# Kernel tuning notes

Measured on AMD Instinct MI355X. Metric: run time of the kernel, lower is better.

The kernel has to match this reference:

```python
import jax, jax.numpy as jnp
import numpy as np
from jax import lax

RADII = (0.1, 0.2, 0.4)
NSAMPLES = (16, 32, 128)
MLPS = ((3, 32, 32, 64), (3, 64, 64, 128), (3, 64, 96, 128))  # divide_ratio=1


def fps(xyz, npoint):
    # iterative farthest point sampling; xyz [B,N,3] -> idx [B,npoint]
    B, N, _ = xyz.shape
    def body(carry, _):
        mind, last = carry
        p = jnp.take_along_axis(xyz, last[:, None, None], axis=1)  # [B,1,3]
        d = jnp.sum((xyz - p) ** 2, -1)
        mind = jnp.minimum(mind, d)
        nxt = jnp.argmax(mind, -1).astype(jnp.int32)
        return (mind, nxt), last
    init = (jnp.full((B, N), 1e10, xyz.dtype), jnp.zeros((B,), jnp.int32))
    _, idx = lax.scan(body, init, None, length=npoint)
    return jnp.transpose(idx)  # [B,npoint]


def ball_query(radius, nsample, xyz, new_xyz):
    # first-nsample neighbors within radius; pad with first valid index
    N = xyz.shape[1]
    sq = jnp.sum((new_xyz[:, :, None, :] - xyz[:, None, :, :]) ** 2, -1)  # [B,S,N]
    cand = jnp.where(sq < radius * radius,
                     jnp.arange(N, dtype=jnp.int32)[None, None, :], N)
    idx = jnp.sort(cand, axis=-1)[:, :, :nsample]
    first = idx[:, :, :1]
    return jnp.where(idx == N, first, idx).astype(jnp.int32)


def scale_branch(xyz, new_xyz, radius, nsample, weights):
    idx = ball_query(radius, nsample, xyz, new_xyz)
    grouped = jax.vmap(lambda x, i: x[i])(xyz, idx)          # [B,S,ns,3]
    h = grouped - new_xyz[:, :, None, :]                      # relative coords (points=None)
    for w, b in weights:                                      # shared 1x1-conv MLP
        h = jax.nn.relu(jnp.einsum('bsnc,co->bsno', h, w) + b)
    return jnp.max(h, axis=2)                                 # maxpool over neighbors [B,S,C]


def _forward(pcd, params, wf, bf):
    npoint = pcd.shape[1] // 8
    idx = fps(pcd, npoint)
    new_xyz = jnp.take_along_axis(pcd, idx[:, :, None], axis=1)  # [B,S,3]
    feats = [scale_branch(pcd, new_xyz, RADII[i], NSAMPLES[i], params[i]) for i in range(3)]
    h = jnp.concatenate(feats, axis=-1)                          # [B,S,320]
    return jnp.einsum('bsc,co->bso', h, wf) + bf                 # patch values [B,S,1]


def setup_inputs() -> dict:
    key = jax.random.key(0)
    ks = jax.random.split(key, 32)
    B, N = 8, 4096
    inp = {"pcd": jax.random.uniform(ks[0], (B, N, 3), jnp.float32)}
    ki = 1
    for si, dims in enumerate(MLPS):
        for li in range(3):
            cin, cout = dims[li], dims[li + 1]
            inp[f"w{si}{li}"] = jax.random.normal(ks[ki], (cin, cout), jnp.float32) * (2.0 / cin) ** 0.5
            inp[f"b{si}{li}"] = jnp.zeros((cout,), jnp.float32)
            ki += 1
    inp["wf"] = jax.random.normal(ks[ki], (320, 1), jnp.float32) * 0.05
    inp["bf"] = jnp.zeros((1,), jnp.float32)
    return inp


def reference(pcd, w00, b00, w01, b01, w02, b02,
              w10, b10, w11, b11, w12, b12,
              w20, b20, w21, b21, w22, b22, wf, bf):
    params = [[(w00, b00), (w01, b01), (w02, b02)],
              [(w10, b10), (w11, b11), (w12, b12)],
              [(w20, b20), (w21, b21), (w22, b22)]]
    return _forward(pcd, params, wf, bf)
```

## Files before the change

kernel.cpp:

```cpp
#include <hip/hip_runtime.h>

#define BATCH 8
#define NPTS 4096
#define NSAMP 512

#define ROW_SHR(n) (0x110 | (n))
#define ROW_BCAST15 0x142
#define ROW_BCAST31 0x143

template <int CTRL, int RMASK>
__device__ __forceinline__ float fmax_dpp(float x) {
  int t = __builtin_amdgcn_update_dpp(0, __float_as_int(x), CTRL, RMASK, 0xf, true);
  return fmaxf(x, __int_as_float(t));
}

__device__ __forceinline__ float wave_max(float x) {
  x = fmax_dpp<ROW_SHR(1), 0xf>(x);
  x = fmax_dpp<ROW_SHR(2), 0xf>(x);
  x = fmax_dpp<ROW_SHR(4), 0xf>(x);
  x = fmax_dpp<ROW_SHR(8), 0xf>(x);
  x = fmax_dpp<ROW_BCAST15, 0xa>(x);
  x = fmax_dpp<ROW_BCAST31, 0xc>(x);
  return x;
}

__device__ __forceinline__ void tsec(int g, const float* __restrict__ w,
                                     float* __restrict__ wt, int cin, int cinp,
                                     int cout, int base) {
  int local = g - base;
  if (local < 0 || local >= cinp * cout) return;
  int oc = local / cinp, ic = local % cinp;
  wt[base + local] = (ic < cin) ? w[ic * cout + oc] : 0.0f;
}

#define W00 0
#define W01 128
#define W02 1152
#define W10 3200
#define W11 3456
#define W12 7552
#define W20 15744
#define WT_TOTAL 16000

__global__ __launch_bounds__(256) void prep_kernel(
    const float* w00, const float* w01, const float* w02,
    const float* w10, const float* w11, const float* w12,
    const float* w20, float* __restrict__ wt) {
  int g = blockIdx.x * 256 + threadIdx.x;
  tsec(g, w00, wt, 3, 4, 32, W00);
  tsec(g, w01, wt, 32, 32, 32, W01);
  tsec(g, w02, wt, 32, 32, 64, W02);
  tsec(g, w10, wt, 3, 4, 64, W10);
  tsec(g, w11, wt, 64, 64, 64, W11);
  tsec(g, w12, wt, 64, 64, 128, W12);
  tsec(g, w20, wt, 3, 4, 64, W20);
}

template <int TOC, int TN>
__device__ __forceinline__ void ib(float (&acc)[TOC][TN], const float* bias) {
#pragma unroll
  for (int j = 0; j < TOC; ++j) {
    float bj = bias[j];
#pragma unroll
    for (int i = 0; i < TN; ++i) acc[j][i] = bj;
  }
}

template <int CIN4, int TOC, int TN, int NTPI, int WS>
__device__ __forceinline__ void layer_acc(const float* __restrict__ wtb,
                                          const float* hin,
                                          float (&acc)[TOC][TN], int tn) {
#pragma unroll 2
  for (int c4 = 0; c4 < CIN4; ++c4) {
    float hv[4][TN];
#pragma unroll
    for (int k = 0; k < 4; ++k) {
      const float* src = &hin[(c4 * 4 + k) * NTPI + tn * TN];
      if constexpr (TN == 1) {
        hv[k][0] = src[0];
      } else if constexpr (TN == 2) {
        float2 v = *(const float2*)src; hv[k][0] = v.x; hv[k][1] = v.y;
      } else {
        float4 v = *(const float4*)src;
        hv[k][0] = v.x; hv[k][1] = v.y; hv[k][2] = v.z; hv[k][3] = v.w;
      }
    }
#pragma unroll
    for (int j = 0; j < TOC; ++j) {
      float4 w4 = *(const float4*)&wtb[j * WS + c4 * 4];
#pragma unroll
      for (int i = 0; i < TN; ++i) {
        acc[j][i] = fmaf(hv[0][i], w4.x, acc[j][i]);
        acc[j][i] = fmaf(hv[1][i], w4.y, acc[j][i]);
        acc[j][i] = fmaf(hv[2][i], w4.z, acc[j][i]);
        acc[j][i] = fmaf(hv[3][i], w4.w, acc[j][i]);
      }
    }
  }
}

template <int TOC, int TN, int NTPO>
__device__ __forceinline__ void store_relu(float* hout,
                                           float (&acc)[TOC][TN], int tn) {
#pragma unroll
  for (int j = 0; j < TOC; ++j) {
    float* dst = &hout[j * NTPO + tn * TN];
    if constexpr (TN == 1) {
      dst[0] = fmaxf(acc[j][0], 0.0f);
    } else if constexpr (TN == 2) {
      *(float2*)dst = make_float2(fmaxf(acc[j][0], 0.0f),
                                  fmaxf(acc[j][1], 0.0f));
    } else {
      *(float4*)dst = make_float4(fmaxf(acc[j][0], 0.0f),
                                  fmaxf(acc[j][1], 0.0f),
                                  fmaxf(acc[j][2], 0.0f),
                                  fmaxf(acc[j][3], 0.0f));
    }
  }
}

template <int TOC, int TN>
__device__ __forceinline__ void rmax_upd(float (&r)[TOC],
                                         float (&acc)[TOC][TN]) {
#pragma unroll
  for (int j = 0; j < TOC; ++j) {
    float m = 0.0f;
#pragma unroll
    for (int i = 0; i < TN; ++i) m = fmaxf(m, acc[j][i]);
    r[j] = fmaxf(r[j], m);
  }
}

template <int TOC>
__device__ __forceinline__ void rmax_commit(float* fdst, float (&r)[TOC],
                                            int tn) {
#pragma unroll
  for (int j = 0; j < TOC; ++j) {
    float v = r[j];
    v = fmaxf(v, __shfl_xor(v, 1));
    v = fmaxf(v, __shfl_xor(v, 2));
    v = fmaxf(v, __shfl_xor(v, 4));
    v = fmaxf(v, __shfl_xor(v, 8));
    if (tn == 0) fdst[j] = v;
  }
}

__global__ __launch_bounds__(256) void fused_kernel(
    const float* __restrict__ pcd, float* __restrict__ new_xyz,
    int* __restrict__ ctrl, const float* __restrict__ wt,
    const float* __restrict__ w21o, const float* __restrict__ w22o,
    const float* __restrict__ b00, const float* __restrict__ b01,
    const float* __restrict__ b02, const float* __restrict__ b10,
    const float* __restrict__ b11, const float* __restrict__ b12,
    const float* __restrict__ b20, const float* __restrict__ b21,
    const float* __restrict__ b22,
    const float* __restrict__ wf, const float* __restrict__ bf,
    float* __restrict__ out) {
  __shared__ __align__(16) float lds[11264];
  __shared__ int s_ticket;

  const int tid = threadIdx.x;
  int* progress = ctrl + 8;

  if (tid == 0) s_ticket = atomicAdd(&ctrl[0], 1);
  __syncthreads();
  const int ticket = s_ticket;

  if (ticket < BATCH) {
    const int b = ticket;
    const int t = tid;
    const int wave = t >> 6, lane = t & 63;
    const float* xb = pcd + (size_t)b * NPTS * 3;
    float4* slot = (float4*)lds;

    float X[16], Y[16], Z[16], mind[16];
    {
      float f[48];
      float4* vv = (float4*)f;
      const float4* src = (const float4*)xb + t * 12;
#pragma unroll
      for (int q = 0; q < 12; ++q) vv[q] = src[q];
#pragma unroll
      for (int j = 0; j < 16; ++j) {
        X[j] = f[3 * j + 0]; Y[j] = f[3 * j + 1]; Z[j] = f[3 * j + 2];
        mind[j] = 10000000000.0f;
      }
    }
    float px = xb[0], py = xb[1], pz = xb[2];

    for (int it = 0; it < NSAMP; ++it) {
      if (t == 0) {
        int* dst = (int*)(new_xyz + ((size_t)b * NSAMP + it) * 3);
        atomicExch(&dst[0], __float_as_int(px));
        atomicExch(&dst[1], __float_as_int(py));
        atomicExch(&dst[2], __float_as_int(pz));
        if ((it & 7) == 7)
          __hip_atomic_store(&progress[b], it + 1, __ATOMIC_RELEASE,
                             __HIP_MEMORY_SCOPE_AGENT);
      }
      float bv = -1.0f, bx = 0.0f, by = 0.0f, bz = 0.0f;
#pragma unroll
      for (int j = 0; j < 16; ++j) {
        float dx = __fsub_rn(X[j], px);
        float dy = __fsub_rn(Y[j], py);
        float dz = __fsub_rn(Z[j], pz);
        float d = __fadd_rn(__fadd_rn(__fmul_rn(dx, dx), __fmul_rn(dy, dy)),
                            __fmul_rn(dz, dz));
        float m = fminf(mind[j], d);
        mind[j] = m;
        bool g = m > bv;
        bv = g ? m : bv;
        bx = g ? X[j] : bx; by = g ? Y[j] : by; bz = g ? Z[j] : bz;
      }
      float wmax = __int_as_float(
          __builtin_amdgcn_readlane(__float_as_int(wave_max(bv)), 63));
      unsigned long long msk = __ballot(bv == wmax);
      if (lane == __ffsll(msk) - 1)
        slot[(it & 1) * 4 + wave] = make_float4(bx, by, bz, wmax);
      __syncthreads();
      float4 cur = slot[(it & 1) * 4 + 0];
#pragma unroll
      for (int w = 1; w < 4; ++w) {
        float4 sw = slot[(it & 1) * 4 + w];
        if (sw.w > cur.w) cur = sw;
      }
      px = cur.x; py = cur.y; pz = cur.z;
    }
    return;
  }

  const int tk = ticket - BATCH;
  const int b = tk & 7;
  const int s = tk >> 3;
  const int bs = (b << 9) | s;
  const int lane = tid & 63;
  const int wave = tid >> 6;
  const int tn = tid & 15, toc = tid >> 4;
  const float* xb = pcd + (size_t)b * NPTS * 3;

  float* h1 = lds;
  float* h2 = lds + 4096;
  float* sB = lds + 4096;
  float* sA = lds + 6272;
  float* cbuf  = lds + 10240;
  float* cbuf2 = lds + 10512;
  float* feat = lds + 10784;
  unsigned long long* masks = (unsigned long long*)(lds + 10784);
  unsigned short* gl = (unsigned short*)(lds + 11168);
  float* bc = lds + 11256;

  if (tid == 0) {
    while (__hip_atomic_load(&progress[b], __ATOMIC_ACQUIRE,
                             __HIP_MEMORY_SCOPE_AGENT) <= s)
      __builtin_amdgcn_s_sleep(2);
    const int* src = (const int*)(new_xyz + (size_t)bs * 3);
    bc[0] = __int_as_float(__hip_atomic_load(&src[0], __ATOMIC_RELAXED,
                                             __HIP_MEMORY_SCOPE_AGENT));
    bc[1] = __int_as_float(__hip_atomic_load(&src[1], __ATOMIC_RELAXED,
                                             __HIP_MEMORY_SCOPE_AGENT));
    bc[2] = __int_as_float(__hip_atomic_load(&src[2], __ATOMIC_RELAXED,
                                             __HIP_MEMORY_SCOPE_AGENT));
  }
  __syncthreads();
  const float cx = bc[0], cy = bc[1], cz = bc[2];

  const float r2a = (float)(0.1 * 0.1);
  const float r2b = (float)(0.2 * 0.2);
  const float r2c = (float)(0.4 * 0.4);
#pragma unroll 4
  for (int j = 0; j < 16; ++j) {
    int i = (j << 8) | tid;
    const float* p = xb + i * 3;
    float dx = __fsub_rn(cx, p[0]);
    float dy = __fsub_rn(cy, p[1]);
    float dz = __fsub_rn(cz, p[2]);
    float sq = __fadd_rn(__fadd_rn(__fmul_rn(dx, dx), __fmul_rn(dy, dy)),
                         __fmul_rn(dz, dz));
    unsigned long long m0 = __ballot(sq < r2a);
    unsigned long long m1 = __ballot(sq < r2b);
    unsigned long long m2 = __ballot(sq < r2c);
    if (lane == 0) {
      int c = (j << 2) | wave;
      masks[0 * 64 + c] = m0; masks[1 * 64 + c] = m1; masks[2 * 64 + c] = m2;
    }
  }
  __syncthreads();

  if (wave < 3) {
    const int ns  = (wave == 0) ? 16 : (wave == 1) ? 32 : 128;
    const int off = (wave == 0) ? 0  : (wave == 1) ? 16 : 48;
    unsigned long long m = masks[wave * 64 + lane];
    int pc = (int)__popcll(m);
    int incl = pc;
#pragma unroll
    for (int o = 1; o < 64; o <<= 1) {
      int u = __shfl_up(incl, o);
      if (lane >= o) incl += u;
    }
    int ex = incl - pc;
    int total = __shfl(incl, 63);
    unsigned short* glw = gl + off;
    unsigned long long mm = m;
    int p = ex;
    while (mm && p < ns) {
      int l = (int)__builtin_ctzll(mm);
      mm &= mm - 1;
      glw[p++] = (unsigned short)((lane << 6) | l);
    }
    int cnt = total < ns ? total : ns;
    unsigned long long nz = __ballot(pc > 0);
    int fl = __ffsll(nz) - 1;
    int myf = (lane << 6) | (int)__builtin_ctzll(m | 0x8000000000000000ull);
    int fidx = __shfl(myf, fl);
    for (int k = cnt + lane; k < ns; k += 64) glw[k] = (unsigned short)fidx;
  }
  __syncthreads();

  if (tid < 68) { cbuf[3 * 68 + tid] = 0.0f; cbuf2[3 * 68 + tid] = 0.0f; }
  if (tid < 48) {
    int j = gl[tid];
    const float* p = xb + 3 * j;
    cbuf[0 * 68 + tid] = __fsub_rn(p[0], cx);
    cbuf[1 * 68 + tid] = __fsub_rn(p[1], cy);
    cbuf[2 * 68 + tid] = __fsub_rn(p[2], cz);
  }
  __syncthreads();

  {
    float a[2][1]; ib<2, 1>(a, b00 + toc * 2);
    layer_acc<1, 2, 1, 68, 4>(wt + W00 + (toc * 2) * 4, cbuf, a, tn);
    store_relu<2, 1, 18>(sB + (toc * 2) * 18, a, tn);
  }
  __syncthreads();

  {
    float a[2][1]; ib<2, 1>(a, b01 + toc * 2);
    layer_acc<8, 2, 1, 18, 32>(wt + W01 + (toc * 2) * 32, sB, a, tn);
    store_relu<2, 1, 18>(sA + (toc * 2) * 18, a, tn);
  }
  __syncthreads();

  {
    float a[4][1]; ib<4, 1>(a, b02 + toc * 4);
    layer_acc<8, 4, 1, 18, 32>(wt + W02 + (toc * 4) * 32, sA, a, tn);
    float r[4] = {0.0f, 0.0f, 0.0f, 0.0f};
    rmax_upd<4, 1>(r, a);
    rmax_commit<4>(feat + toc * 4, r, tn);
    float a1[4][2]; ib<4, 2>(a1, b10 + toc * 4);
    layer_acc<1, 4, 2, 68, 4>(wt + W10 + (toc * 4) * 4, cbuf + 16, a1, tn);
    store_relu<4, 2, 34>(sB + (toc * 4) * 34, a1, tn);
  }
  __syncthreads();

  {
    float a[4][2]; ib<4, 2>(a, b11 + toc * 4);
    layer_acc<16, 4, 2, 34, 64>(wt + W11 + (toc * 4) * 64, sB, a, tn);
    store_relu<4, 2, 34>(sA + (toc * 4) * 34, a, tn);
    if (tid < 64) {
      int j = gl[48 + tid];
      const float* p = xb + 3 * j;
      cbuf[0 * 68 + tid] = __fsub_rn(p[0], cx);
      cbuf[1 * 68 + tid] = __fsub_rn(p[1], cy);
      cbuf[2 * 68 + tid] = __fsub_rn(p[2], cz);
    }
  }
  __syncthreads();

  {
    float a[8][2]; ib<8, 2>(a, b12 + toc * 8);
    layer_acc<16, 8, 2, 34, 64>(wt + W12 + (toc * 8) * 64, sA, a, tn);
    float r[8] = {0.0f, 0.0f, 0.0f, 0.0f, 0.0f, 0.0f, 0.0f, 0.0f};
    rmax_upd<8, 2>(r, a);
    rmax_commit<8>(feat + 64 + toc * 8, r, tn);
    float a2[4][4]; ib<4, 4>(a2, b20 + toc * 4);
    layer_acc<1, 4, 4, 68, 4>(wt + W20 + (toc * 4) * 4, cbuf, a2, tn);
    store_relu<4, 4, 64>(h1 + (toc * 4) * 64, a2, tn);
  }
  __syncthreads();

  const int wq = __builtin_amdgcn_readfirstlane(wave);
  float rm2[32];
#pragma unroll
  for (int j = 0; j < 32; ++j) rm2[j] = 0.0f;

  {
    if (tid < 64) {
      int j = gl[112 + tid];
      const float* p = xb + 3 * j;
      cbuf2[0 * 68 + tid] = __fsub_rn(p[0], cx);
      cbuf2[1 * 68 + tid] = __fsub_rn(p[1], cy);
      cbuf2[2 * 68 + tid] = __fsub_rn(p[2], cz);
    }
    const float* wp = w21o + wq * 24;
    const float* bp = b21 + wq * 24;
    float acc[24];
#pragma unroll
    for (int j = 0; j < 24; ++j) acc[j] = bp[j];
#pragma unroll 4
    for (int k = 0; k < 64; ++k) {
      float hv = h1[k * 64 + lane];
#pragma unroll
      for (int j = 0; j < 24; ++j) acc[j] = fmaf(hv, wp[k * 96 + j], acc[j]);
    }
#pragma unroll
    for (int j = 0; j < 24; ++j)
      h2[(wq * 24 + j) * 64 + lane] = fmaxf(acc[j], 0.0f);
  }
  __syncthreads();

  {
    float a2[4][4]; ib<4, 4>(a2, b20 + toc * 4);
    layer_acc<1, 4, 4, 68, 4>(wt + W20 + (toc * 4) * 4, cbuf2, a2, tn);
    store_relu<4, 4, 64>(h1 + (toc * 4) * 64, a2, tn);
    const float* wp = w22o + wq * 32;
    const float* bp = b22 + wq * 32;
    float acc[32];
#pragma unroll
    for (int j = 0; j < 32; ++j) acc[j] = bp[j];
#pragma unroll 2
    for (int k = 0; k < 96; ++k) {
      float hv = h2[k * 64 + lane];
#pragma unroll
      for (int j = 0; j < 32; ++j) acc[j] = fmaf(hv, wp[k * 128 + j], acc[j]);
    }
#pragma unroll
    for (int j = 0; j < 32; ++j) rm2[j] = fmaxf(rm2[j], fmaxf(acc[j], 0.0f));
  }
  __syncthreads();

  {
    const float* wp = w21o + wq * 24;
    const float* bp = b21 + wq * 24;
    float acc[24];
#pragma unroll
    for (int j = 0; j < 24; ++j) acc[j] = bp[j];
#pragma unroll 4
    for (int k = 0; k < 64; ++k) {
      float hv = h1[k * 64 + lane];
#pragma unroll
      for (int j = 0; j < 24; ++j) acc[j] = fmaf(hv, wp[k * 96 + j], acc[j]);
    }
#pragma unroll
    for (int j = 0; j < 24; ++j)
      h2[(wq * 24 + j) * 64 + lane] = fmaxf(acc[j], 0.0f);
  }
  __syncthreads();

  {
    const float* wp = w22o + wq * 32;
    const float* bp = b22 + wq * 32;
    float acc[32];
#pragma unroll
    for (int j = 0; j < 32; ++j) acc[j] = bp[j];
#pragma unroll 2
    for (int k = 0; k < 96; ++k) {
      float hv = h2[k * 64 + lane];
#pragma unroll
      for (int j = 0; j < 32; ++j) acc[j] = fmaf(hv, wp[k * 128 + j], acc[j]);
    }
#pragma unroll
    for (int j = 0; j < 32; ++j) {
      float v = fmaxf(rm2[j], fmaxf(acc[j], 0.0f));
      v = wave_max(v);
      if (lane == 63) feat[192 + wq * 32 + j] = v;
    }
  }
  __syncthreads();

  if (tid < 64) {
    float sacc = 0.0f;
#pragma unroll
    for (int c = 0; c < 5; ++c) sacc += feat[tid + c * 64] * wf[tid + c * 64];
#pragma unroll
    for (int o = 32; o > 0; o >>= 1) sacc += __shfl_down(sacc, o);
    if (tid == 0) out[bs] = sacc + bf[0];
  }
}

extern "C" void kernel_launch(void* const* d_in, const int* in_sizes, int n_in,
                              void* d_out, int out_size, void* d_ws, size_t ws_size,
                              hipStream_t stream) {
  const float* pcd = (const float*)d_in[0];
  float* wsf = (float*)d_ws;
  float* new_xyz = wsf;
  float* wt = wsf + 12288;
  int* ctrl = (int*)(wsf + 28288);

  hipMemsetAsync(ctrl, 0, 64, stream);

  prep_kernel<<<(WT_TOTAL + 255) / 256, 256, 0, stream>>>(
      (const float*)d_in[1], (const float*)d_in[3], (const float*)d_in[5],
      (const float*)d_in[7], (const float*)d_in[9], (const float*)d_in[11],
      (const float*)d_in[13], wt);

  fused_kernel<<<BATCH * NSAMP + BATCH, 256, 0, stream>>>(
      pcd, new_xyz, ctrl, wt,
      (const float*)d_in[15], (const float*)d_in[17],
      (const float*)d_in[2],  (const float*)d_in[4],  (const float*)d_in[6],
      (const float*)d_in[8],  (const float*)d_in[10], (const float*)d_in[12],
      (const float*)d_in[14], (const float*)d_in[16], (const float*)d_in[18],
      (const float*)d_in[19], (const float*)d_in[20],
      (float*)d_out);
}
```

Measured before the change: 504.1 us.

## Compute scale-2 first layer per-lane and fuse final projection into max-pool reduction

The first layer of scale branch 2 (3->64) now runs per lane straight from the original weights, each lane gathering its own neighbor point into registers. This removes the transposed W20 prep section and the cbuf2 staging buffer. The final 320->1 projection is folded into each max-pool reduction as a running dot product and reduced across waves at the end, which drops the feat buffer and one barrier. LDS shrinks from about 45 KB to 40 KB, which may allow higher occupancy, at the cost of extra global loads of uncached weights per lane.

```diff
diff --git a/kernel.cpp b/kernel.cpp
--- a/kernel.cpp
+++ b/kernel.cpp
@@ -39,13 +39,12 @@
 #define W10 3200
 #define W11 3456
 #define W12 7552
-#define W20 15744
-#define WT_TOTAL 16000
+#define WT_TOTAL 15744
 
 __global__ __launch_bounds__(256) void prep_kernel(
     const float* w00, const float* w01, const float* w02,
     const float* w10, const float* w11, const float* w12,
-    const float* w20, float* __restrict__ wt) {
+    float* __restrict__ wt) {
   int g = blockIdx.x * 256 + threadIdx.x;
   tsec(g, w00, wt, 3, 4, 32, W00);
   tsec(g, w01, wt, 32, 32, 32, W01);
@@ -53,7 +52,6 @@
   tsec(g, w10, wt, 3, 4, 64, W10);
   tsec(g, w11, wt, 64, 64, 64, W11);
   tsec(g, w12, wt, 64, 64, 128, W12);
-  tsec(g, w20, wt, 3, 4, 64, W20);
 }
 
 template <int TOC, int TN>
@@ -120,35 +118,28 @@
 }
 
 template <int TOC, int TN>
-__device__ __forceinline__ void rmax_upd(float (&r)[TOC],
-                                         float (&acc)[TOC][TN]) {
+__device__ __forceinline__ float rmax_dot(const float* wfp,
+                                          float (&acc)[TOC][TN], int tn) {
+  float s = 0.0f;
 #pragma unroll
   for (int j = 0; j < TOC; ++j) {
-    float m = 0.0f;
-#pragma unroll
-    for (int i = 0; i < TN; ++i) m = fmaxf(m, acc[j][i]);
-    r[j] = fmaxf(r[j], m);
-  }
-}
-
-template <int TOC>
-__device__ __forceinline__ void rmax_commit(float* fdst, float (&r)[TOC],
-                                            int tn) {
-#pragma unroll
-  for (int j = 0; j < TOC; ++j) {
-    float v = r[j];
+    float v = 0.0f;
+#pragma unroll
+    for (int i = 0; i < TN; ++i) v = fmaxf(v, acc[j][i]);
     v = fmaxf(v, __shfl_xor(v, 1));
     v = fmaxf(v, __shfl_xor(v, 2));
     v = fmaxf(v, __shfl_xor(v, 4));
     v = fmaxf(v, __shfl_xor(v, 8));
-    if (tn == 0) fdst[j] = v;
-  }
+    if (tn == 0) s = fmaf(v, wfp[j], s);
+  }
+  return s;
 }
 
 __global__ __launch_bounds__(256) void fused_kernel(
     const float* __restrict__ pcd, float* __restrict__ new_xyz,
     int* __restrict__ ctrl, const float* __restrict__ wt,
-    const float* __restrict__ w21o, const float* __restrict__ w22o,
+    const float* __restrict__ w20o, const float* __restrict__ w21o,
+    const float* __restrict__ w22o,
     const float* __restrict__ b00, const float* __restrict__ b01,
     const float* __restrict__ b02, const float* __restrict__ b10,
     const float* __restrict__ b11, const float* __restrict__ b12,
@@ -156,22 +147,21 @@
     const float* __restrict__ b22,
     const float* __restrict__ wf, const float* __restrict__ bf,
     float* __restrict__ out) {
-  __shared__ __align__(16) float lds[11264];
-  __shared__ int s_ticket;
+  __shared__ __align__(16) float lds[10240];
 
   const int tid = threadIdx.x;
   int* progress = ctrl + 8;
 
-  if (tid == 0) s_ticket = atomicAdd(&ctrl[0], 1);
-  __syncthreads();
-  const int ticket = s_ticket;
+  if (tid == 0) ((int*)lds)[0] = atomicAdd(&ctrl[0], 1);
+  __syncthreads();
+  const int ticket = ((int*)lds)[0];
 
   if (ticket < BATCH) {
     const int b = ticket;
     const int t = tid;
     const int wave = t >> 6, lane = t & 63;
     const float* xb = pcd + (size_t)b * NPTS * 3;
-    float4* slot = (float4*)lds;
+    float4* slot = (float4*)(lds + 16);
 
     float X[16], Y[16], Z[16], mind[16];
     {
@@ -242,12 +232,11 @@
   float* h2 = lds + 4096;
   float* sB = lds + 4096;
   float* sA = lds + 6272;
-  float* cbuf  = lds + 10240;
-  float* cbuf2 = lds + 10512;
-  float* feat = lds + 10784;
-  unsigned long long* masks = (unsigned long long*)(lds + 10784);
-  unsigned short* gl = (unsigned short*)(lds + 11168);
-  float* bc = lds + 11256;
+  float* cbuf = lds + 8448;
+  unsigned short* gl = (unsigned short*)(lds + 8720);
+  float* bc = lds + 4;
+  float* wsum = lds + 8;
+  unsigned long long* masks = (unsigned long long*)(lds + 64);
 
   if (tid == 0) {
     while (__hip_atomic_load(&progress[b], __ATOMIC_ACQUIRE,
@@ -316,7 +305,7 @@
   }
   __syncthreads();
 
-  if (tid < 68) { cbuf[3 * 68 + tid] = 0.0f; cbuf2[3 * 68 + tid] = 0.0f; }
+  if (tid < 68) cbuf[3 * 68 + tid] = 0.0f;
   if (tid < 48) {
     int j = gl[tid];
     const float* p = xb + 3 * j;
@@ -324,7 +313,12 @@
     cbuf[1 * 68 + tid] = __fsub_rn(p[1], cy);
     cbuf[2 * 68 + tid] = __fsub_rn(p[2], cz);
   }
-  __syncthreads();
+  const int gi0 = gl[48 + lane];
+  const int gi1 = gl[112 + lane];
+  __syncthreads();
+
+  const int wq = __builtin_amdgcn_readfirstlane(wave);
+  float dot = 0.0f;
 
   {
     float a[2][1]; ib<2, 1>(a, b00 + toc * 2);
@@ -343,9 +337,7 @@
   {
     float a[4][1]; ib<4, 1>(a, b02 + toc * 4);
     layer_acc<8, 4, 1, 18, 32>(wt + W02 + (toc * 4) * 32, sA, a, tn);
-    float r[4] = {0.0f, 0.0f, 0.0f, 0.0f};
-    rmax_upd<4, 1>(r, a);
-    rmax_commit<4>(feat + toc * 4, r, tn);
+    dot += rmax_dot<4, 1>(wf + toc * 4, a, tn);
     float a1[4][2]; ib<4, 2>(a1, b10 + toc * 4);
     layer_acc<1, 4, 2, 68, 4>(wt + W10 + (toc * 4) * 4, cbuf + 16, a1, tn);
     store_relu<4, 2, 34>(sB + (toc * 4) * 34, a1, tn);
@@ -356,41 +348,35 @@
     float a[4][2]; ib<4, 2>(a, b11 + toc * 4);
     layer_acc<16, 4, 2, 34, 64>(wt + W11 + (toc * 4) * 64, sB, a, tn);
     store_relu<4, 2, 34>(sA + (toc * 4) * 34, a, tn);
-    if (tid < 64) {
-      int j = gl[48 + tid];
-      const float* p = xb + 3 * j;
-      cbuf[0 * 68 + tid] = __fsub_rn(p[0], cx);
-      cbuf[1 * 68 + tid] = __fsub_rn(p[1], cy);
-      cbuf[2 * 68 + tid] = __fsub_rn(p[2], cz);
-    }
   }
   __syncthreads();
 
   {
     float a[8][2]; ib<8, 2>(a, b12 + toc * 8);
     layer_acc<16, 8, 2, 34, 64>(wt + W12 + (toc * 8) * 64, sA, a, tn);
-    float r[8] = {0.0f, 0.0f, 0.0f, 0.0f, 0.0f, 0.0f, 0.0f, 0.0f};
-    rmax_upd<8, 2>(r, a);
-    rmax_commit<8>(feat + 64 + toc * 8, r, tn);
-    float a2[4][4]; ib<4, 4>(a2, b20 + toc * 4);
-    layer_acc<1, 4, 4, 68, 4>(wt + W20 + (toc * 4) * 4, cbuf, a2, tn);
-    store_relu<4, 4, 64>(h1 + (toc * 4) * 64, a2, tn);
-  }
-  __syncthreads();
-
-  const int wq = __builtin_amdgcn_readfirstlane(wave);
+    dot += rmax_dot<8, 2>(wf + 64 + toc * 8, a, tn);
+    const float* p = xb + 3 * gi0;
+    float dx = __fsub_rn(p[0], cx);
+    float dy = __fsub_rn(p[1], cy);
+    float dz = __fsub_rn(p[2], cz);
+    const float* wp = w20o + wq * 16;
+    const float* bp = b20 + wq * 16;
+#pragma unroll
+    for (int j = 0; j < 16; ++j) {
+      float a2 = bp[j];
+      a2 = fmaf(dx, wp[0 * 64 + j], a2);
+      a2 = fmaf(dy, wp[1 * 64 + j], a2);
+      a2 = fmaf(dz, wp[2 * 64 + j], a2);
+      h1[(wq * 16 + j) * 64 + lane] = fmaxf(a2, 0.0f);
+    }
+  }
+  __syncthreads();
+
   float rm2[32];
 #pragma unroll
   for (int j = 0; j < 32; ++j) rm2[j] = 0.0f;
 
   {
-    if (tid < 64) {
-      int j = gl[112 + tid];
-      const float* p = xb + 3 * j;
-      cbuf2[0 * 68 + tid] = __fsub_rn(p[0], cx);
-      cbuf2[1 * 68 + tid] = __fsub_rn(p[1], cy);
-      cbuf2[2 * 68 + tid] = __fsub_rn(p[2], cz);
-    }
     const float* wp = w21o + wq * 24;
     const float* bp = b21 + wq * 24;
     float acc[24];
@@ -409,9 +395,20 @@
   __syncthreads();
 
   {
-    float a2[4][4]; ib<4, 4>(a2, b20 + toc * 4);
-    layer_acc<1, 4, 4, 68, 4>(wt + W20 + (toc * 4) * 4, cbuf2, a2, tn);
-    store_relu<4, 4, 64>(h1 + (toc * 4) * 64, a2, tn);
+    const float* p = xb + 3 * gi1;
+    float dx = __fsub_rn(p[0], cx);
+    float dy = __fsub_rn(p[1], cy);
+    float dz = __fsub_rn(p[2], cz);
+    const float* wp0 = w20o + wq * 16;
+    const float* bp0 = b20 + wq * 16;
+#pragma unroll
+    for (int j = 0; j < 16; ++j) {
+      float a2 = bp0[j];
+      a2 = fmaf(dx, wp0[0 * 64 + j], a2);
+      a2 = fmaf(dy, wp0[1 * 64 + j], a2);
+      a2 = fmaf(dz, wp0[2 * 64 + j], a2);
+      h1[(wq * 16 + j) * 64 + lane] = fmaxf(a2, 0.0f);
+    }
     const float* wp = w22o + wq * 32;
     const float* bp = b22 + wq * 32;
     float acc[32];
@@ -462,19 +459,16 @@
     for (int j = 0; j < 32; ++j) {
       float v = fmaxf(rm2[j], fmaxf(acc[j], 0.0f));
       v = wave_max(v);
-      if (lane == 63) feat[192 + wq * 32 + j] = v;
-    }
-  }
-  __syncthreads();
-
-  if (tid < 64) {
-    float sacc = 0.0f;
-#pragma unroll
-    for (int c = 0; c < 5; ++c) sacc += feat[tid + c * 64] * wf[tid + c * 64];
-#pragma unroll
-    for (int o = 32; o > 0; o >>= 1) sacc += __shfl_down(sacc, o);
-    if (tid == 0) out[bs] = sacc + bf[0];
-  }
+      if (lane == 63) dot = fmaf(v, wf[192 + wq * 32 + j], dot);
+    }
+  }
+
+#pragma unroll
+  for (int o = 1; o < 64; o <<= 1) dot += __shfl_xor(dot, o);
+  if (lane == 0) wsum[wq] = dot;
+  __syncthreads();
+  if (tid == 0)
+    out[bs] = wsum[0] + wsum[1] + wsum[2] + wsum[3] + bf[0];
 }
 
 extern "C" void kernel_launch(void* const* d_in, const int* in_sizes, int n_in,
@@ -491,11 +485,11 @@
   prep_kernel<<<(WT_TOTAL + 255) / 256, 256, 0, stream>>>(
       (const float*)d_in[1], (const float*)d_in[3], (const float*)d_in[5],
       (const float*)d_in[7], (const float*)d_in[9], (const float*)d_in[11],
-      (const float*)d_in[13], wt);
+      wt);
 
   fused_kernel<<<BATCH * NSAMP + BATCH, 256, 0, stream>>>(
       pcd, new_xyz, ctrl, wt,
-      (const float*)d_in[15], (const float*)d_in[17],
+      (const float*)d_in[13], (const float*)d_in[15], (const float*)d_in[17],
       (const float*)d_in[2],  (const float*)d_in[4],  (const float*)d_in[6],
       (const float*)d_in[8],  (const float*)d_in[10], (const float*)d_in[12],
       (const float*)d_in[14], (const float*)d_in[16], (const float*)d_in[18],
```

Result: no change. 510.9 us (+1.4%).
